# Performance work log

Hardware: AMD Instinct MI355X
Metric: run time of the kernel (lower is better)

Reference implementation:

```python
import jax, jax.numpy as jnp
import numpy as np

LGRAD = 27.8   # gradient scale (module _lgrad)
LCOL = 10.0    # color scale   (module _lcol)
MAXLVL = 4     # merge levels  (module _maxlvl)
FINAL_TH = 0.0 # merge threshold (module _final_th)


def _grad_mag(feat):
    # per-pixel gradient magnitude, averaged over channels -> [B,H,W]
    gx = jnp.pad(feat[..., :, 1:] - feat[..., :, :-1], ((0, 0), (0, 0), (0, 0), (0, 1)))
    gy = jnp.pad(feat[..., 1:, :] - feat[..., :-1, :], ((0, 0), (0, 0), (0, 1), (0, 0)))
    return jnp.sqrt(gx * gx + gy * gy + 1e-12).mean(axis=1)


def _edges(H, W):
    # directed 4-connectivity edge list over the pixel grid (static, numpy)
    idx = np.arange(H * W).reshape(H, W)
    hu, hv = idx[:, :-1].ravel(), idx[:, 1:].ravel()
    vu, vv = idx[:-1, :].ravel(), idx[1:, :].ravel()
    src = np.concatenate([hu, hv, vu, vv]).astype(np.int32)
    dst = np.concatenate([hv, hu, vv, vu]).astype(np.int32)
    return jnp.asarray(src), jnp.asarray(dst)


def _merge_level(labels, pix, gmag, src, dst, N):
    # labels [N] int32 pixel->region, pix [N,3], gmag [N]
    ones = jnp.ones_like(gmag)
    cnt = jax.ops.segment_sum(ones, labels, num_segments=N)
    csum = jax.ops.segment_sum(pix, labels, num_segments=N)
    gsum = jax.ops.segment_sum(gmag, labels, num_segments=N)
    safe = jnp.maximum(cnt, 1.0)
    mcol = csum / safe[:, None]      # region mean color [N,3]
    mg = gsum / safe                 # region mean gradient [N]

    la, lb = labels[src], labels[dst]
    valid = la != lb
    dc = jnp.sqrt(jnp.sum((mcol[la] - mcol[lb]) ** 2, axis=-1) + 1e-12)
    ge = 0.5 * (mg[la] + mg[lb])
    sim = jnp.exp(-(dc / LCOL + ge / LGRAD))     # in (0,1], higher = more similar
    sim = jnp.where(valid, sim, -1.0)

    best = jax.ops.segment_max(sim, la, num_segments=N)     # best-neighbor similarity
    cand = jnp.where(valid & (sim == best[la]), lb, jnp.int32(N))
    bn = jax.ops.segment_min(cand, la, num_segments=N)      # deterministic best neighbor id

    r = jnp.arange(N, dtype=jnp.int32)
    bnc = jnp.clip(bn, 0, N - 1)
    mutual = (bn < N) & (bnc[bnc] == r) & (best > FINAL_TH)  # mutual-best, cycle-free pairs
    parent = jnp.where(mutual, jnp.minimum(r, bnc), r)
    return parent[labels]


def _tokenize(feat):
    B, C, H, W = feat.shape
    N = H * W
    gmag = _grad_mag(feat).reshape(B, N)
    pix = feat.reshape(B, C, N).transpose(0, 2, 1)            # [B,N,3]
    src, dst = _edges(H, W)
    labels = jnp.broadcast_to(jnp.arange(N, dtype=jnp.int32), (B, N))

    step = jax.vmap(lambda l, p, g: _merge_level(l, p, g, src, dst, N))
    for _ in range(MAXLVL):
        labels = step(labels, pix, gmag)

    def mean_map(l, p):
        cnt = jax.ops.segment_sum(jnp.ones((N,), p.dtype), l, num_segments=N)
        cs = jax.ops.segment_sum(p, l, num_segments=N)
        return (cs / jnp.maximum(cnt, 1.0)[:, None])[l]

    colmap = jax.vmap(mean_map)(labels, pix)                  # [B,N,3] region-mean colors
    colmap = colmap.transpose(0, 2, 1).reshape(B, C, H, W)
    return labels.reshape(B, H, W), colmap


def setup_inputs() -> dict:
    key = jax.random.key(0)
    feat = jax.random.uniform(key, (8, 3, 512, 512), dtype=jnp.float32) * 255.0
    return {"feat": feat}


def reference(feat):
    return _tokenize(feat)
```

## Files before the change

kernel.cpp:

```cpp
#include <hip/hip_runtime.h>
#include <math.h>

#define WW 512
#define HH 512
#define NPIX (WW*HH)
#define NSH 18
#define NXCD 8

typedef unsigned long long u64;
typedef unsigned int u32;
typedef unsigned short u16;

__device__ __forceinline__ u64 umax64(u64 a, u64 b) { return a > b ? a : b; }

__device__ __forceinline__ int swz_idx() {
  int g = gridDim.x;
  int b = (int)blockIdx.x;
  int nb2 = (b & (NXCD - 1)) * (g >> 3) + (b >> 3);
  return nb2 * 256 + (int)threadIdx.x;
}

__device__ __forceinline__ void tile_coords(int& bb, int& x0, int& y0) {
  int g = gridDim.x;
  int b = (int)blockIdx.x;
  int t = (b & (NXCD - 1)) * (g >> 3) + (b >> 3);
  bb = t >> 10;
  int rem = t & 1023;
  y0 = (rem >> 4) << 3;
  x0 = (rem & 15) << 5;
}

__device__ __forceinline__ float d_colg(const float* __restrict__ fb, int p, int pw, int ph,
                                        float col[3]) {
  float s = 0.f;
#pragma unroll
  for (int c = 0; c < 3; ++c) {
    const float* fc = fb + (size_t)c * NPIX;
    float v = fc[p];
    col[c] = v;
    float gx = (pw < WW - 1) ? __fsub_rn(fc[p + 1], v) : 0.f;
    float gy = (ph < HH - 1) ? __fsub_rn(fc[p + WW], v) : 0.f;
    float g = __fsqrt_rn(__fadd_rn(__fadd_rn(__fmul_rn(gx, gx), __fmul_rn(gy, gy)), 1e-12f));
    s = __fadd_rn(s, g);
  }
  return __fdiv_rn(s, 3.0f);
}

__device__ __forceinline__ u64 d_simbits(float4 a, float4 b) {
  float d0 = __fsub_rn(a.x, b.x);
  float d1 = __fsub_rn(a.y, b.y);
  float d2 = __fsub_rn(a.z, b.z);
  float ss = __fadd_rn(__fadd_rn(__fmul_rn(d0, d0), __fmul_rn(d1, d1)), __fmul_rn(d2, d2));
  float dc = __fsqrt_rn(__fadd_rn(ss, 1e-12f));
  float ge = __fmul_rn(0.5f, __fadd_rn(a.w, b.w));
  float t = __fadd_rn(__fdiv_rn(dc, 10.0f), __fdiv_rn(ge, 27.8f));
  float sim = (float)exp(-(double)t);
  return ((u64)__float_as_uint(sim)) << 32;
}

__global__ __launch_bounds__(256) void k_prep0edge(const float* __restrict__ feat,
                                                   int* __restrict__ labels,
                                                   int* __restrict__ cnt,
                                                   float4* __restrict__ pix4,
                                                   float4* __restrict__ mcol4,
                                                   u64* __restrict__ bnkey) {
  __shared__ float4 scolg[340];
  __shared__ u64 skey[256];
  int bb, x0, y0;
  tile_coords(bb, x0, y0);
  const float* fb = feat + (size_t)bb * 3 * NPIX;
  int tid = (int)threadIdx.x;
  skey[tid] = 0;
  for (int c = tid; c < 340; c += 256) {
    int cx = (c % 34) - 1, cy = (c / 34) - 1;
    int x = x0 + cx, y = y0 + cy;
    if (x >= 0 && x < WW && y >= 0 && y < HH) {
      float col[3];
      float g = d_colg(fb, y * WW + x, x, y, col);
      scolg[c] = make_float4(col[0], col[1], col[2], g);
    }
  }
  __syncthreads();
  int tx = tid & 31, ty = tid >> 5;
  int x = x0 + tx, y = y0 + ty;
  int n = y * WW + x;
  int idx = (bb << NSH) + n;
  int cell = (ty + 1) * 34 + (tx + 1);
  float4 ca = scolg[cell];
  labels[idx] = n;
  cnt[idx] = 1;
  pix4[idx] = ca;
  mcol4[idx] = ca;
  u64 key = 0;
  if (x < WW - 1) {
    u64 s = d_simbits(ca, scolg[cell + 1]);
    key = umax64(key, s | (u32)(NPIX - (n + 1)));
    if (tx < 31) atomicMax(&skey[tid + 1], s | (u32)(NPIX - n));
  }
  if (tx == 0 && x > 0) {
    u64 s = d_simbits(ca, scolg[cell - 1]);
    key = umax64(key, s | (u32)(NPIX - (n - 1)));
  }
  if (y < HH - 1) {
    u64 s = d_simbits(ca, scolg[cell + 34]);
    key = umax64(key, s | (u32)(NPIX - (n + WW)));
    if (ty < 7) atomicMax(&skey[tid + 32], s | (u32)(NPIX - n));
  }
  if (ty == 0 && y > 0) {
    u64 s = d_simbits(ca, scolg[cell - 34]);
    key = umax64(key, s | (u32)(NPIX - (n - WW)));
  }
  __syncthreads();
  bnkey[idx] = umax64(key, skey[tid]);
}

__global__ __launch_bounds__(256) void k_edge(const int* __restrict__ labels,
                                              const float4* __restrict__ mcol4,
                                              u64* __restrict__ bnkey, int lvl) {
  __shared__ int sla[256];
  __shared__ float4 sma[256];
  __shared__ u64 skey[256];
  int bb, x0, y0;
  tile_coords(bb, x0, y0);
  int tid = (int)threadIdx.x;
  int tx = tid & 31, ty = tid >> 5;
  int x = x0 + tx, y = y0 + ty;
  int n = y * WW + x;
  int base = bb << NSH;
  int idx = base + n;
  int la = labels[idx];
  float4 ma = mcol4[base + la];
  sla[tid] = la;
  sma[tid] = ma;
  skey[tid] = 0;
  __syncthreads();
  u64 key = 0;
  if (x < WW - 1) {
    if (tx < 31) {
      int lb = sla[tid + 1];
      if (lb != la) {
        u64 s = d_simbits(ma, sma[tid + 1]);
        key = umax64(key, s | (u32)(NPIX - lb));
        atomicMax(&skey[tid + 1], s | (u32)(NPIX - la));
      }
    } else {
      int lb = labels[idx + 1];
      if (lb != la) key = umax64(key, d_simbits(ma, mcol4[base + lb]) | (u32)(NPIX - lb));
    }
  }
  if (tx == 0 && x > 0) {
    int lb = labels[idx - 1];
    if (lb != la) key = umax64(key, d_simbits(ma, mcol4[base + lb]) | (u32)(NPIX - lb));
  }
  if (y < HH - 1) {
    if (ty < 7) {
      int lb = sla[tid + 32];
      if (lb != la) {
        u64 s = d_simbits(ma, sma[tid + 32]);
        key = umax64(key, s | (u32)(NPIX - lb));
        atomicMax(&skey[tid + 32], s | (u32)(NPIX - la));
      }
    } else {
      int lb = labels[idx + WW];
      if (lb != la) key = umax64(key, d_simbits(ma, mcol4[base + lb]) | (u32)(NPIX - lb));
    }
  }
  if (ty == 0 && y > 0) {
    int lb = labels[idx - WW];
    if (lb != la) key = umax64(key, d_simbits(ma, mcol4[base + lb]) | (u32)(NPIX - lb));
  }
  __syncthreads();
  u64 val = umax64(key, skey[tid]);
  skey[tid] = val;
  __syncthreads();
  bool leader = (tx == 0) || (sla[tid - 1] != la);
  if (leader) {
    u64 m = val;
    int t = tid + 1, txx = tx + 1;
    while (txx < 32 && sla[t] == la) { m = umax64(m, skey[t]); ++t; ++txx; }
    if (m) atomicMax(&bnkey[base + la], ((u64)lvl << 62) | m);
  }
}

template<bool LVL0, bool LAST>
__global__ __launch_bounds__(256) void k_scanpairs(int* __restrict__ labels,
                                                   int* __restrict__ cnt,
                                                   u16* __restrict__ mem,
                                                   const u64* __restrict__ bnkey,
                                                   const float4* __restrict__ pix4,
                                                   float4* __restrict__ mcol4,
                                                   int total, int lvl) {
  __shared__ u64 swl[256];
  __shared__ int scnt;
  if (threadIdx.x == 0) scnt = 0;
  __syncthreads();

  int idx = swz_idx();
  bool pred = false;
  u64 e = 0;
  if (idx < total) {
    int n = idx & (NPIX - 1);
    int base = idx - n;
    u64 K = bnkey[idx];
    bool valid = LVL0 ? true : ((int)(K >> 62) == lvl);
    if (valid) {
      int v = NPIX - (int)(K & 0xffffffffu);
      if (v < NPIX && n < v) {
        u64 Kv = bnkey[base + v];
        bool pv = LVL0 ? true : ((int)(Kv >> 62) == lvl);
        if (pv && NPIX - (int)(Kv & 0xffffffffu) == n) {
          pred = true;
          e = ((u64)(u32)idx << 32) | (u32)v;
        }
      }
    }
  }

  u64 mask = __ballot(pred);
  int lane = (int)(threadIdx.x & 63);
  int wb0 = 0;
  if (lane == 0 && mask) wb0 = atomicAdd(&scnt, __popcll(mask));
  int wb = __shfl(wb0, 0);
  if (pred) {
    int pos = wb + __popcll(mask & ((1ull << lane) - 1ull));
    swl[pos] = e;
  }
  __syncthreads();
  int m = scnt;
  if ((int)threadIdx.x >= m) return;

  e = swl[threadIdx.x];
  int idx2 = (int)(e >> 32);
  int v = (int)(e & 0xffffffffu);
  int n = idx2 & (NPIX - 1);
  int base = idx2 - n;
  u16* mo = mem + ((size_t)idx2 << 4);
  if (LVL0) {
    float4 pa = pix4[idx2];
    float4 pb = pix4[base + v];
    float s0 = __fadd_rn(__fadd_rn(0.f, pa.x), pb.x);
    float s1 = __fadd_rn(__fadd_rn(0.f, pa.y), pb.y);
    float s2 = __fadd_rn(__fadd_rn(0.f, pa.z), pb.z);
    float sg = __fadd_rn(__fadd_rn(0.f, pa.w), pb.w);
    mo[0] = 0; mo[1] = (u16)(v - n);
    labels[base + v] = n;
    mcol4[idx2] = make_float4(__fdiv_rn(s0, 2.0f), __fdiv_rn(s1, 2.0f),
                              __fdiv_rn(s2, 2.0f), __fdiv_rn(sg, 2.0f));
    cnt[idx2] = 2;
    cnt[base + v] = 0;
  } else {
    int c = cnt[idx2];
    int cb = cnt[base + v];
    const u16* ma = mem + ((size_t)idx2 << 4);
    const u16* mb = mem + ((size_t)(base + v) << 4);
    int k = c + cb;
    float s0 = 0.f, s1 = 0.f, s2 = 0.f, sg = 0.f;
    int i = 0, j = 0;
    while (i < c || j < cb) {
      int av = (i < c) ? ((c == 1) ? n : n + (int)ma[i]) : 0x7fffffff;
      int bv = (j < cb) ? ((cb == 1) ? v : v + (int)mb[j]) : 0x7fffffff;
      int x;
      bool fromB;
      if (av < bv) { x = av; ++i; fromB = false; } else { x = bv; ++j; fromB = true; }
      float4 p = pix4[base + x];
      s0 = __fadd_rn(s0, p.x);
      s1 = __fadd_rn(s1, p.y);
      s2 = __fadd_rn(s2, p.z);
      sg = __fadd_rn(sg, p.w);
      if (!LAST && fromB) labels[base + x] = n;
    }
    if (!LAST) {
      int i2 = c - 1, j2 = cb - 1;
      for (int t2 = k - 1; t2 >= 0; --t2) {
        int av = (i2 >= 0) ? ((c == 1) ? n : n + (int)ma[i2]) : (int)0x80000000;
        int bv = (j2 >= 0) ? ((cb == 1) ? v : v + (int)mb[j2]) : (int)0x80000000;
        int x;
        if (av > bv) { x = av; --i2; } else { x = bv; --j2; }
        mo[t2] = (u16)(x - n);
      }
    }
    float safe = (float)k;
    mcol4[idx2] = make_float4(__fdiv_rn(s0, safe), __fdiv_rn(s1, safe),
                              __fdiv_rn(s2, safe), __fdiv_rn(sg, safe));
    if (LAST) {
      cnt[base + v] = -n;
    } else {
      cnt[idx2] = k;
      cnt[base + v] = 0;
    }
  }
}

__global__ __launch_bounds__(256) void k_out(const int* __restrict__ labels,
                                             const int* __restrict__ cnt,
                                             const float4* __restrict__ mcol4,
                                             float* __restrict__ out, int total,
                                             int b0, int Btot) {
  int idx = swz_idx();
  if (idx >= total) return;
  int b = idx >> NSH;
  int n = idx & (NPIX - 1);
  int base = b << NSH;
  int l = labels[idx];
  int c2 = cnt[base + l];
  if (c2 <= 0) l = -c2;
  out[(size_t)(b0 + b) * NPIX + n] = (float)l;
  size_t cb = (size_t)Btot * NPIX;
  float4 m = mcol4[base + l];
  out[cb + ((size_t)(b0 + b) * 3 + 0) * NPIX + n] = m.x;
  out[cb + ((size_t)(b0 + b) * 3 + 1) * NPIX + n] = m.y;
  out[cb + ((size_t)(b0 + b) * 3 + 2) * NPIX + n] = m.z;
}

extern "C" void kernel_launch(void* const* d_in, const int* in_sizes, int n_in,
                              void* d_out, int out_size, void* d_ws, size_t ws_size,
                              hipStream_t stream) {
  const float* feat = (const float*)d_in[0];
  float* out = (float*)d_out;
  int Btot = in_sizes[0] / (3 * NPIX);

  const size_t perB = (size_t)NPIX * 80;
  int nbmax = (int)(ws_size / perB);
  if (nbmax < 1) nbmax = 1;
  if (nbmax > Btot) nbmax = Btot;

  for (int b0 = 0; b0 < Btot; b0 += nbmax) {
    int nb = (Btot - b0 < nbmax) ? (Btot - b0) : nbmax;
    size_t cn = (size_t)nb << NSH;
    char* p = (char*)d_ws;
    float4* mcol4 = (float4*)p; p += cn * 16;
    float4* pix4 = (float4*)p;  p += cn * 16;
    u64* key = (u64*)p;         p += cn * 8;
    int* labels = (int*)p;      p += cn * 4;
    int* cnt = (int*)p;         p += cn * 4;
    u16* mem = (u16*)p;

    const float* fchunk = feat + (size_t)b0 * 3 * NPIX;
    int total = (int)cn;
    int grid = total >> 8;

    k_prep0edge<<<grid, 256, 0, stream>>>(fchunk, labels, cnt, pix4, mcol4, key);
    k_scanpairs<true, false><<<grid, 256, 0, stream>>>(labels, cnt, mem, key,
                                                       pix4, mcol4, total, 0);
    k_edge<<<grid, 256, 0, stream>>>(labels, mcol4, key, 1);
    k_scanpairs<false, false><<<grid, 256, 0, stream>>>(labels, cnt, mem, key,
                                                        pix4, mcol4, total, 1);
    k_edge<<<grid, 256, 0, stream>>>(labels, mcol4, key, 2);
    k_scanpairs<false, false><<<grid, 256, 0, stream>>>(labels, cnt, mem, key,
                                                        pix4, mcol4, total, 2);
    k_edge<<<grid, 256, 0, stream>>>(labels, mcol4, key, 3);
    k_scanpairs<false, true><<<grid, 256, 0, stream>>>(labels, cnt, mem, key,
                                                       pix4, mcol4, total, 3);
    k_out<<<grid, 256, 0, stream>>>(labels, cnt, mcol4, out, total, b0, Btot);
  }
}
```

Measured before the change: 258.5 us.

## Fuse level-0 mutual-pair merge into prep kernel via 2-pixel halo

Widens the prep tile's shared-memory halo from 1 to 2 pixels so each thread can recompute its best neighbor's best-neighbor key locally. Level-0 mutual-pair detection and the pair merge (mean color, labels, counts, member list) now happen inside the prep kernel. This removes a separate level-0 scan kernel launch and its global reads and compaction. In exchange it adds redundant similarity evaluations (exp in double) for neighbors that fall in the halo, plus a larger halo load.

```diff
diff --git a/kernel.cpp b/kernel.cpp
--- a/kernel.cpp
+++ b/kernel.cpp
@@ -58,21 +58,22 @@
   return ((u64)__float_as_uint(sim)) << 32;
 }
 
-__global__ __launch_bounds__(256) void k_prep0edge(const float* __restrict__ feat,
-                                                   int* __restrict__ labels,
-                                                   int* __restrict__ cnt,
-                                                   float4* __restrict__ pix4,
-                                                   float4* __restrict__ mcol4,
-                                                   u64* __restrict__ bnkey) {
-  __shared__ float4 scolg[340];
+__global__ __launch_bounds__(256) void k_prep0(const float* __restrict__ feat,
+                                               int* __restrict__ labels,
+                                               int* __restrict__ cnt,
+                                               float4* __restrict__ pix4,
+                                               float4* __restrict__ mcol4,
+                                               u16* __restrict__ mem,
+                                               u64* __restrict__ bnkey) {
+  __shared__ float4 scolg[432];
   __shared__ u64 skey[256];
   int bb, x0, y0;
   tile_coords(bb, x0, y0);
   const float* fb = feat + (size_t)bb * 3 * NPIX;
   int tid = (int)threadIdx.x;
   skey[tid] = 0;
-  for (int c = tid; c < 340; c += 256) {
-    int cx = (c % 34) - 1, cy = (c / 34) - 1;
+  for (int c = tid; c < 432; c += 256) {
+    int cx = (c % 36) - 2, cy = (c / 36) - 2;
     int x = x0 + cx, y = y0 + cy;
     if (x >= 0 && x < WW && y >= 0 && y < HH) {
       float col[3];
@@ -85,33 +86,68 @@
   int x = x0 + tx, y = y0 + ty;
   int n = y * WW + x;
   int idx = (bb << NSH) + n;
-  int cell = (ty + 1) * 34 + (tx + 1);
-  float4 ca = scolg[cell];
-  labels[idx] = n;
-  cnt[idx] = 1;
+  int cc = (ty + 2) * 36 + (tx + 2);
+  float4 ca = scolg[cc];
   pix4[idx] = ca;
-  mcol4[idx] = ca;
   u64 key = 0;
   if (x < WW - 1) {
-    u64 s = d_simbits(ca, scolg[cell + 1]);
+    u64 s = d_simbits(ca, scolg[cc + 1]);
     key = umax64(key, s | (u32)(NPIX - (n + 1)));
     if (tx < 31) atomicMax(&skey[tid + 1], s | (u32)(NPIX - n));
   }
-  if (tx == 0 && x > 0) {
-    u64 s = d_simbits(ca, scolg[cell - 1]);
-    key = umax64(key, s | (u32)(NPIX - (n - 1)));
-  }
+  if (tx == 0 && x > 0)
+    key = umax64(key, d_simbits(ca, scolg[cc - 1]) | (u32)(NPIX - (n - 1)));
   if (y < HH - 1) {
-    u64 s = d_simbits(ca, scolg[cell + 34]);
+    u64 s = d_simbits(ca, scolg[cc + 36]);
     key = umax64(key, s | (u32)(NPIX - (n + WW)));
     if (ty < 7) atomicMax(&skey[tid + 32], s | (u32)(NPIX - n));
   }
-  if (ty == 0 && y > 0) {
-    u64 s = d_simbits(ca, scolg[cell - 34]);
-    key = umax64(key, s | (u32)(NPIX - (n - WW)));
-  }
-  __syncthreads();
-  bnkey[idx] = umax64(key, skey[tid]);
+  if (ty == 0 && y > 0)
+    key = umax64(key, d_simbits(ca, scolg[cc - 36]) | (u32)(NPIX - (n - WW)));
+  __syncthreads();
+  key = umax64(key, skey[tid]);
+  bnkey[idx] = key;
+  skey[tid] = key;
+  __syncthreads();
+
+  int v = NPIX - (int)(key & 0xffffffffu);
+  int vx = v & (WW - 1), vy = v >> 9;
+  u64 kv;
+  if (vx >= x0 && vx < x0 + 32 && vy >= y0 && vy < y0 + 8) {
+    kv = skey[(vy - y0) * 32 + (vx - x0)];
+  } else {
+    int vc = (vy - y0 + 2) * 36 + (vx - x0 + 2);
+    float4 cv = scolg[vc];
+    kv = 0;
+    if (vx < WW - 1) kv = umax64(kv, d_simbits(cv, scolg[vc + 1]) | (u32)(NPIX - (v + 1)));
+    if (vx > 0)      kv = umax64(kv, d_simbits(cv, scolg[vc - 1]) | (u32)(NPIX - (v - 1)));
+    if (vy < HH - 1) kv = umax64(kv, d_simbits(cv, scolg[vc + 36]) | (u32)(NPIX - (v + WW)));
+    if (vy > 0)      kv = umax64(kv, d_simbits(cv, scolg[vc - 36]) | (u32)(NPIX - (v - WW)));
+  }
+  bool mutual = (NPIX - (int)(kv & 0xffffffffu)) == n;
+  if (mutual) {
+    if (n < v) {
+      float4 pb = scolg[(vy - y0 + 2) * 36 + (vx - x0 + 2)];
+      float s0 = __fadd_rn(__fadd_rn(0.f, ca.x), pb.x);
+      float s1 = __fadd_rn(__fadd_rn(0.f, ca.y), pb.y);
+      float s2 = __fadd_rn(__fadd_rn(0.f, ca.z), pb.z);
+      float sg = __fadd_rn(__fadd_rn(0.f, ca.w), pb.w);
+      mcol4[idx] = make_float4(__fdiv_rn(s0, 2.0f), __fdiv_rn(s1, 2.0f),
+                               __fdiv_rn(s2, 2.0f), __fdiv_rn(sg, 2.0f));
+      labels[idx] = n;
+      cnt[idx] = 2;
+      u16* mo = mem + ((size_t)idx << 4);
+      mo[0] = 0; mo[1] = (u16)(v - n);
+    } else {
+      labels[idx] = v;
+      cnt[idx] = 0;
+      mcol4[idx] = ca;
+    }
+  } else {
+    labels[idx] = n;
+    cnt[idx] = 1;
+    mcol4[idx] = ca;
+  }
 }
 
 __global__ __launch_bounds__(256) void k_edge(const int* __restrict__ labels,
@@ -182,7 +218,7 @@
   }
 }
 
-template<bool LVL0, bool LAST>
+template<bool LAST>
 __global__ __launch_bounds__(256) void k_scanpairs(int* __restrict__ labels,
                                                    int* __restrict__ cnt,
                                                    u16* __restrict__ mem,
@@ -202,13 +238,11 @@
     int n = idx & (NPIX - 1);
     int base = idx - n;
     u64 K = bnkey[idx];
-    bool valid = LVL0 ? true : ((int)(K >> 62) == lvl);
-    if (valid) {
+    if ((int)(K >> 62) == lvl) {
       int v = NPIX - (int)(K & 0xffffffffu);
       if (v < NPIX && n < v) {
         u64 Kv = bnkey[base + v];
-        bool pv = LVL0 ? true : ((int)(Kv >> 62) == lvl);
-        if (pv && NPIX - (int)(Kv & 0xffffffffu) == n) {
+        if ((int)(Kv >> 62) == lvl && NPIX - (int)(Kv & 0xffffffffu) == n) {
           pred = true;
           e = ((u64)(u32)idx << 32) | (u32)v;
         }
@@ -235,59 +269,44 @@
   int n = idx2 & (NPIX - 1);
   int base = idx2 - n;
   u16* mo = mem + ((size_t)idx2 << 4);
-  if (LVL0) {
-    float4 pa = pix4[idx2];
-    float4 pb = pix4[base + v];
-    float s0 = __fadd_rn(__fadd_rn(0.f, pa.x), pb.x);
-    float s1 = __fadd_rn(__fadd_rn(0.f, pa.y), pb.y);
-    float s2 = __fadd_rn(__fadd_rn(0.f, pa.z), pb.z);
-    float sg = __fadd_rn(__fadd_rn(0.f, pa.w), pb.w);
-    mo[0] = 0; mo[1] = (u16)(v - n);
-    labels[base + v] = n;
-    mcol4[idx2] = make_float4(__fdiv_rn(s0, 2.0f), __fdiv_rn(s1, 2.0f),
-                              __fdiv_rn(s2, 2.0f), __fdiv_rn(sg, 2.0f));
-    cnt[idx2] = 2;
+  int c = cnt[idx2];
+  int cb = cnt[base + v];
+  const u16* ma = mem + ((size_t)idx2 << 4);
+  const u16* mb = mem + ((size_t)(base + v) << 4);
+  int k = c + cb;
+  float s0 = 0.f, s1 = 0.f, s2 = 0.f, sg = 0.f;
+  int i = 0, j = 0;
+  while (i < c || j < cb) {
+    int av = (i < c) ? ((c == 1) ? n : n + (int)ma[i]) : 0x7fffffff;
+    int bv = (j < cb) ? ((cb == 1) ? v : v + (int)mb[j]) : 0x7fffffff;
+    int x;
+    bool fromB;
+    if (av < bv) { x = av; ++i; fromB = false; } else { x = bv; ++j; fromB = true; }
+    float4 p = pix4[base + x];
+    s0 = __fadd_rn(s0, p.x);
+    s1 = __fadd_rn(s1, p.y);
+    s2 = __fadd_rn(s2, p.z);
+    sg = __fadd_rn(sg, p.w);
+    if (!LAST && fromB) labels[base + x] = n;
+  }
+  if (!LAST) {
+    int i2 = c - 1, j2 = cb - 1;
+    for (int t2 = k - 1; t2 >= 0; --t2) {
+      int av = (i2 >= 0) ? ((c == 1) ? n : n + (int)ma[i2]) : (int)0x80000000;
+      int bv = (j2 >= 0) ? ((cb == 1) ? v : v + (int)mb[j2]) : (int)0x80000000;
+      int x;
+      if (av > bv) { x = av; --i2; } else { x = bv; --j2; }
+      mo[t2] = (u16)(x - n);
+    }
+  }
+  float safe = (float)k;
+  mcol4[idx2] = make_float4(__fdiv_rn(s0, safe), __fdiv_rn(s1, safe),
+                            __fdiv_rn(s2, safe), __fdiv_rn(sg, safe));
+  if (LAST) {
+    cnt[base + v] = -n;
+  } else {
+    cnt[idx2] = k;
     cnt[base + v] = 0;
-  } else {
-    int c = cnt[idx2];
-    int cb = cnt[base + v];
-    const u16* ma = mem + ((size_t)idx2 << 4);
-    const u16* mb = mem + ((size_t)(base + v) << 4);
-    int k = c + cb;
-    float s0 = 0.f, s1 = 0.f, s2 = 0.f, sg = 0.f;
-    int i = 0, j = 0;
-    while (i < c || j < cb) {
-      int av = (i < c) ? ((c == 1) ? n : n + (int)ma[i]) : 0x7fffffff;
-      int bv = (j < cb) ? ((cb == 1) ? v : v + (int)mb[j]) : 0x7fffffff;
-      int x;
-      bool fromB;
-      if (av < bv) { x = av; ++i; fromB = false; } else { x = bv; ++j; fromB = true; }
-      float4 p = pix4[base + x];
-      s0 = __fadd_rn(s0, p.x);
-      s1 = __fadd_rn(s1, p.y);
-      s2 = __fadd_rn(s2, p.z);
-      sg = __fadd_rn(sg, p.w);
-      if (!LAST && fromB) labels[base + x] = n;
-    }
-    if (!LAST) {
-      int i2 = c - 1, j2 = cb - 1;
-      for (int t2 = k - 1; t2 >= 0; --t2) {
-        int av = (i2 >= 0) ? ((c == 1) ? n : n + (int)ma[i2]) : (int)0x80000000;
-        int bv = (j2 >= 0) ? ((cb == 1) ? v : v + (int)mb[j2]) : (int)0x80000000;
-        int x;
-        if (av > bv) { x = av; --i2; } else { x = bv; --j2; }
-        mo[t2] = (u16)(x - n);
-      }
-    }
-    float safe = (float)k;
-    mcol4[idx2] = make_float4(__fdiv_rn(s0, safe), __fdiv_rn(s1, safe),
-                              __fdiv_rn(s2, safe), __fdiv_rn(sg, safe));
-    if (LAST) {
-      cnt[base + v] = -n;
-    } else {
-      cnt[idx2] = k;
-      cnt[base + v] = 0;
-    }
   }
 }
 
@@ -339,18 +358,16 @@
     int total = (int)cn;
     int grid = total >> 8;
 
-    k_prep0edge<<<grid, 256, 0, stream>>>(fchunk, labels, cnt, pix4, mcol4, key);
-    k_scanpairs<true, false><<<grid, 256, 0, stream>>>(labels, cnt, mem, key,
-                                                       pix4, mcol4, total, 0);
+    k_prep0<<<grid, 256, 0, stream>>>(fchunk, labels, cnt, pix4, mcol4, mem, key);
     k_edge<<<grid, 256, 0, stream>>>(labels, mcol4, key, 1);
-    k_scanpairs<false, false><<<grid, 256, 0, stream>>>(labels, cnt, mem, key,
-                                                        pix4, mcol4, total, 1);
+    k_scanpairs<false><<<grid, 256, 0, stream>>>(labels, cnt, mem, key,
+                                                 pix4, mcol4, total, 1);
     k_edge<<<grid, 256, 0, stream>>>(labels, mcol4, key, 2);
-    k_scanpairs<false, false><<<grid, 256, 0, stream>>>(labels, cnt, mem, key,
-                                                        pix4, mcol4, total, 2);
+    k_scanpairs<false><<<grid, 256, 0, stream>>>(labels, cnt, mem, key,
+                                                 pix4, mcol4, total, 2);
     k_edge<<<grid, 256, 0, stream>>>(labels, mcol4, key, 3);
-    k_scanpairs<false, true><<<grid, 256, 0, stream>>>(labels, cnt, mem, key,
-                                                       pix4, mcol4, total, 3);
+    k_scanpairs<true><<<grid, 256, 0, stream>>>(labels, cnt, mem, key,
+                                                pix4, mcol4, total, 3);
     k_out<<<grid, 256, 0, stream>>>(labels, cnt, mcol4, out, total, b0, Btot);
   }
 }
```

New measurement: 250.4 us (median of 2 runs). 1.03x faster.
